# Kernel optimization log

Measured on AMD Instinct MI355X. Metric: run time of the kernel, lower is better.

Reference implementation:

```python
import jax, jax.numpy as jnp
import numpy as np

BN_EPS = 1e-5

def _batchnorm(x):
    # BatchNorm1d(affine=False) in training mode: per-feature batch stats, biased var
    mu = jnp.mean(x, axis=0, keepdims=True)
    var = jnp.mean((x - mu) ** 2, axis=0, keepdims=True)
    return (x - mu) / jnp.sqrt(var + BN_EPS)

def setup_inputs() -> dict:
    key = jax.random.key(0)
    ks = jax.random.split(key, 8)
    H, I, S, E = 1024, 4096, 128, 16384  # hidden, intermediate, sqrt(experts), experts
    std = 0.02
    return {
        "hidden_states": jax.random.normal(ks[0], (4, 2048, H), jnp.float32),
        "gate_proj_weight": jax.random.normal(ks[1], (I, H), jnp.float32) * std,
        "up_proj_weight": jax.random.normal(ks[2], (I, H), jnp.float32) * std,
        "down_proj_weight": jax.random.normal(ks[3], (H, I), jnp.float32) * std,
        "router_gate_x_weight": jax.random.normal(ks[4], (S, H), jnp.float32) * std,
        "router_gate_y_weight": jax.random.normal(ks[5], (S, H), jnp.float32) * std,
        "up_embed": jax.random.normal(ks[6], (E, H), jnp.float32) * std,
        "down_embed": jax.random.normal(ks[7], (E, H), jnp.float32) * std,
        "top_k": 16,
    }

def reference(hidden_states, gate_proj_weight, up_proj_weight, down_proj_weight,
              router_gate_x_weight, router_gate_y_weight, up_embed, down_embed, top_k):
    bsz, seq_len, H = hidden_states.shape
    x = hidden_states.reshape(-1, H)  # [T, H]
    S = router_gate_x_weight.shape[0]  # num_expert_sqrt

    # dual-axis router: two small gates -> batchnorm -> log-softmax
    lpx = jax.nn.log_softmax(_batchnorm(x @ router_gate_x_weight.T), axis=-1)  # [T, S]
    lpy = jax.nn.log_softmax(_batchnorm(x @ router_gate_y_weight.T), axis=-1)  # [T, S]
    # combined log-prob over S*S experts: expert (i,j) -> i*S + j
    combined = (lpx[:, :, None] + lpy[:, None, :]).reshape(-1, S * S)  # [T, S*S]
    scores, indices = jax.lax.top_k(combined, top_k)  # [T, K]
    routing_weights = jnp.exp(scores)  # [T, K] = p_x * p_y

    # embedding-based expert: gather up/down rows, dot-scale-combine
    ue = up_embed[indices]    # [T, K, H]
    de = down_embed[indices]  # [T, K, H]
    up_score = jnp.einsum('tkh,th->tk', ue, x)          # per-expert scalar
    experts_states = jnp.einsum('tk,tkh->th', routing_weights * up_score, de)

    # dense SwiGLU MLP branch
    mlp = (jax.nn.silu(x @ gate_proj_weight.T) * (x @ up_proj_weight.T)) @ down_proj_weight.T

    out = mlp + experts_states
    return out.reshape(bsz, seq_len, H)
```

## Files before the change

### kernel.cpp

```cpp
#include <hip/hip_runtime.h>
#include <hip/hip_bf16.h>
#include <math.h>

#define T_TOK 8192
#define HDIM  1024
#define IDIM  4096
#define SDIM  128
#define TOPK  16

typedef __bf16 bf16x8 __attribute__((ext_vector_type(8)));
typedef float  f32x4  __attribute__((ext_vector_type(4)));

__device__ __forceinline__ unsigned short f2bf(float f) {
    union { float f; unsigned u; } a; a.f = f;
    unsigned r = a.u + 0x7fffu + ((a.u >> 16) & 1u);
    return (unsigned short)(r >> 16);
}
__device__ __forceinline__ float bf2f(unsigned short b) {
    union { unsigned u; float f; } a; a.u = ((unsigned)b) << 16;
    return a.f;
}

__device__ __forceinline__ void gld_lds16(const void* g, void* l) {
    __builtin_amdgcn_global_load_lds(
        (__attribute__((address_space(1))) void*)g,
        (__attribute__((address_space(3))) void*)l,
        16, 0, 0);
}

struct CvtSegs {
    const float4* src[8];
    ushort4*      dst[8];
    int           end[8];
};

__global__ __launch_bounds__(256)
void cvt_all_kernel(CvtSegs segs) {
    int i = blockIdx.x * 256 + threadIdx.x;
    if (i >= segs.end[7]) return;
    int s = 0;
    #pragma unroll
    for (int k = 0; k < 7; ++k) s += (i >= segs.end[k]) ? 1 : 0;
    int base = (s == 0) ? 0 : segs.end[s - 1];
    int j = i - base;
    float4 v = segs.src[s][j];
    ushort4 o;
    o.x = f2bf(v.x); o.y = f2bf(v.y); o.z = f2bf(v.z); o.w = f2bf(v.w);
    segs.dst[s][j] = o;
}

template<int ADD>
__global__ __launch_bounds__(256)
void gemm_bt(const unsigned short* __restrict__ A, const unsigned short* __restrict__ B,
             float* __restrict__ C, int M, int N, int K) {
    __shared__ unsigned short As[4096];
    __shared__ unsigned short Bs[4096];
    const int tid  = threadIdx.x;
    const int lane = tid & 63;
    const int wave = tid >> 6;
    const int tm = blockIdx.x * 128;
    const int tn = blockIdx.y * 128;
    const int wm = (wave & 1) * 64;
    const int wn = (wave >> 1) * 64;
    const int quad = lane >> 4;
    const int tr   = lane & 15;

    f32x4 acc[4][4] = {};
    bf16x8 af[4], bfr[4];

    const int ua0 = tid,        am0 = ua0 & 127, ak0 = ua0 >> 7;
    const int ua1 = tid + 256,  am1 = ua1 & 127, ak1 = ua1 >> 7;

    auto issue = [&](int kt) {
        gld_lds16(A + (size_t)(tm + am0) * K + kt + ak0 * 8, &As[ua0 * 8]);
        gld_lds16(A + (size_t)(tm + am1) * K + kt + ak1 * 8, &As[ua1 * 8]);
        gld_lds16(B + (size_t)(tn + am0) * K + kt + ak0 * 8, &Bs[ua0 * 8]);
        gld_lds16(B + (size_t)(tn + am1) * K + kt + ak1 * 8, &Bs[ua1 * 8]);
    };
    auto rdfrags = [&]() {
        #pragma unroll
        for (int mi = 0; mi < 4; ++mi)
            af[mi] = *(const bf16x8*)&As[(quad * 128 + wm + mi * 16 + tr) * 8];
        #pragma unroll
        for (int ni = 0; ni < 4; ++ni)
            bfr[ni] = *(const bf16x8*)&Bs[(quad * 128 + wn + ni * 16 + tr) * 8];
    };
    auto mfmas = [&]() {
        #pragma unroll
        for (int mi = 0; mi < 4; ++mi)
            #pragma unroll
            for (int ni = 0; ni < 4; ++ni)
                acc[mi][ni] = __builtin_amdgcn_mfma_f32_16x16x32_bf16(af[mi], bfr[ni], acc[mi][ni], 0, 0, 0);
    };

    issue(0);
    asm volatile("s_waitcnt vmcnt(0)" ::: "memory");
    __syncthreads();
    rdfrags();
    for (int kt = 32; kt < K; kt += 32) {
        __syncthreads();
        issue(kt);
        mfmas();
        asm volatile("s_waitcnt vmcnt(0)" ::: "memory");
        __syncthreads();
        rdfrags();
    }
    mfmas();

    #pragma unroll
    for (int mi = 0; mi < 4; ++mi) {
        #pragma unroll
        for (int ni = 0; ni < 4; ++ni) {
            int col = tn + wn + ni * 16 + tr;
            #pragma unroll
            for (int r = 0; r < 4; ++r) {
                int row = tm + wm + mi * 16 + quad * 4 + r;
                size_t o = (size_t)row * N + col;
                float v = acc[mi][ni][r];
                if (ADD) v += C[o];
                C[o] = v;
            }
        }
    }
}

#define BARX() asm volatile("s_barrier" ::: "memory")
#define VMW4() asm volatile("s_waitcnt vmcnt(4)" ::: "memory")
#define VMW3() asm volatile("s_waitcnt vmcnt(3)" ::: "memory")

#define RD_A(par, ks, MB) { const char* _p = lds + ((par) << 15) + ((ks) << 14); \
    af[0] = *(const bf16x8*)(_p + aoff[(MB)+0]); \
    af[1] = *(const bf16x8*)(_p + aoff[(MB)+1]); \
    af[2] = *(const bf16x8*)(_p + aoff[(MB)+2]); \
    af[3] = *(const bf16x8*)(_p + aoff[(MB)+3]); }

#define RD_B(par, ks) { const char* _p = lds + 65536 + ((par) << 15) + ((ks) << 14); \
    bfv[0] = *(const bf16x8*)(_p + boff[0]); \
    bfv[1] = *(const bf16x8*)(_p + boff[1]); \
    bfv[2] = *(const bf16x8*)(_p + boff[2]); \
    bfv[3] = *(const bf16x8*)(_p + boff[3]); }

#define MMA16(ACC) { __builtin_amdgcn_s_setprio(1); \
    _Pragma("unroll") \
    for (int _i = 0; _i < 4; ++_i) \
        _Pragma("unroll") \
        for (int _n = 0; _n < 4; ++_n) \
            ACC[_i][_n] = __builtin_amdgcn_mfma_f32_16x16x32_bf16(af[_i], bfv[_n], ACC[_i][_n], 0, 0, 0); \
    __builtin_amdgcn_s_setprio(0); }

__global__ __launch_bounds__(512, 2)
void gemm1_8ph(const unsigned short* __restrict__ Xb, const unsigned short* __restrict__ Wg,
               const unsigned short* __restrict__ Wu, unsigned short* __restrict__ Hb) {
    __shared__ __align__(16) char lds[131072];
    const int tid  = threadIdx.x;
    const int lane = tid & 63;
    const int wid  = tid >> 6;
    const int quad = lane >> 4;
    const int tr   = lane & 15;
    const int wm   = (wid >> 2) << 7;
    const int wn   = (wid & 3) << 6;

    const int bid = blockIdx.x;
    const int swz = (bid & 7) * 128 + (bid >> 3);
    const int gm  = (swz & 31) << 8;
    const int gn  = (swz >> 5) << 8;

    const int vsw  = (tid & 7) ^ ((tid >> 3) & 7);
    const int rowb = ((tid >> 3) << 1) | (vsw >> 2);
    const int cq8  = (vsw & 3) << 3;

    const unsigned short* pA0 = Xb + (size_t)(gm + rowb) * HDIM + cq8;
    const unsigned short* pA1 = pA0 + (size_t)128 * HDIM;
    auto wsrc = [&](int R) -> const unsigned short* {
        const unsigned short* base = ((R >> 4) & 1) ? Wu : Wg;
        int sr = ((R >> 5) << 4) | (R & 15);
        return base + (size_t)sr * HDIM + cq8;
    };
    const unsigned short* pB0 = wsrc(gn + rowb);
    const unsigned short* pB1 = wsrc(gn + rowb + 128);

    int aoff[8], boff[4];
    #pragma unroll
    for (int i = 0; i < 8; ++i) {
        int row = wm + i * 16 + tr;
        aoff[i] = ((row >> 1) << 7) | (((((row & 1) << 2) | quad) ^ ((row >> 1) & 7)) << 4);
    }
    #pragma unroll
    for (int i = 0; i < 4; ++i) {
        int row = wn + i * 16 + tr;
        boff[i] = ((row >> 1) << 7) | (((((row & 1) << 2) | quad) ^ ((row >> 1) & 7)) << 4);
    }

    f32x4 accL[4][4] = {};
    f32x4 accH[4][4] = {};
    bf16x8 af[4], bfv[4];

    auto stageA = [&](int nxt, int ks, int kOff) {
        char* d = lds + (nxt << 15) + (ks << 14) + (tid << 4);
        gld_lds16(pA0 + kOff, d);
        gld_lds16(pA1 + kOff, d + 8192);
    };
    auto stageB = [&](int nxt, int ks, int kOff) {
        char* d = lds + 65536 + (nxt << 15) + (ks << 14) + (tid << 4);
        gld_lds16(pB0 + kOff, d);
        gld_lds16(pB1 + kOff, d + 8192);
    };

    stageA(0, 0, 0);  stageB(0, 0, 0);
    stageA(0, 1, 32); stageB(0, 1, 32);
    asm volatile("s_waitcnt vmcnt(0)" ::: "memory");
    BARX();

    for (int t = 0; t < 16; ++t) {
        const int par = t & 1, nxt = par ^ 1;
        const int kN = (t < 15 ? t + 1 : 15) << 6;
        RD_A(par, 0, 0); RD_B(par, 0);
        stageA(nxt, 0, kN);
        BARX();
        MMA16(accL);
        BARX();
        RD_A(par, 0, 4);
        stageB(nxt, 0, kN);
        VMW4(); BARX();
        MMA16(accH);
        BARX();
        RD_A(par, 1, 0); RD_B(par, 1);
        stageA(nxt, 1, kN + 32);
        BARX();
        MMA16(accL);
        BARX();
        RD_A(par, 1, 4);
        stageB(nxt, 1, kN + 32);
        VMW4(); BARX();
        MMA16(accH);
        BARX();
    }
    asm volatile("s_waitcnt vmcnt(0)" ::: "memory");

    const size_t icb = (size_t)((gn + wn) >> 1) + tr;
    const int rbase = gm + wm + quad * 4;
    #pragma unroll
    for (int mi = 0; mi < 4; ++mi) {
        #pragma unroll
        for (int p = 0; p < 2; ++p) {
            #pragma unroll
            for (int r = 0; r < 4; ++r) {
                {
                    float g = accL[mi][2 * p][r], u = accL[mi][2 * p + 1][r];
                    float h = g / (1.0f + __expf(-g)) * u;
                    Hb[(size_t)(rbase + mi * 16 + r) * IDIM + icb + 16 * p] = f2bf(h);
                }
                {
                    float g = accH[mi][2 * p][r], u = accH[mi][2 * p + 1][r];
                    float h = g / (1.0f + __expf(-g)) * u;
                    Hb[(size_t)(rbase + 64 + mi * 16 + r) * IDIM + icb + 16 * p] = f2bf(h);
                }
            }
        }
    }
}

#define RD2_A(par, ks) { const char* _p = lds + ((par) << 15) + ((ks) << 14); \
    _Pragma("unroll") \
    for (int _i = 0; _i < 8; ++_i) af[_i] = *(const bf16x8*)(_p + aoff[_i]); }

#define RD2_B(par, ks) { const char* _p = lds + 65536 + ((par) << 14) + ((ks) << 13); \
    bfv[0] = *(const bf16x8*)(_p + boff[0]); \
    bfv[1] = *(const bf16x8*)(_p + boff[1]); }

#define MMA2() { __builtin_amdgcn_s_setprio(1); \
    _Pragma("unroll") \
    for (int _i = 0; _i < 8; ++_i) \
        _Pragma("unroll") \
        for (int _n = 0; _n < 2; ++_n) \
            acc[_i][_n] = __builtin_amdgcn_mfma_f32_16x16x32_bf16(af[_i], bfv[_n], acc[_i][_n], 0, 0, 0); \
    __builtin_amdgcn_s_setprio(0); }

__global__ __launch_bounds__(512, 2)
void gemm2_8ph(const unsigned short* __restrict__ A, const unsigned short* __restrict__ B,
               float* __restrict__ C) {
    __shared__ __align__(16) char lds[98304];
    const int K = IDIM, N = HDIM;
    const int tid  = threadIdx.x;
    const int lane = tid & 63;
    const int wid  = tid >> 6;
    const int quad = lane >> 4;
    const int tr   = lane & 15;
    const int wm   = (wid >> 2) << 7;
    const int wn   = (wid & 3) << 5;

    const int bid = blockIdx.x;
    const int swz = (bid & 7) * 32 + (bid >> 3);
    const int gm  = (swz & 31) << 8;
    const int gn  = (swz >> 5) << 7;

    const int vsw  = (tid & 7) ^ ((tid >> 3) & 7);
    const int rowb = ((tid >> 3) << 1) | (vsw >> 2);
    const int cq8  = (vsw & 3) << 3;

    const unsigned short* pA0 = A + (size_t)(gm + rowb) * K + cq8;
    const unsigned short* pA1 = pA0 + (size_t)128 * K;
    const unsigned short* pB0 = B + (size_t)(gn + rowb) * K + cq8;

    int aoff[8], boff[2];
    #pragma unroll
    for (int i = 0; i < 8; ++i) {
        int row = wm + i * 16 + tr;
        aoff[i] = ((row >> 1) << 7) | (((((row & 1) << 2) | quad) ^ ((row >> 1) & 7)) << 4);
    }
    #pragma unroll
    for (int i = 0; i < 2; ++i) {
        int row = wn + i * 16 + tr;
        boff[i] = ((row >> 1) << 7) | (((((row & 1) << 2) | quad) ^ ((row >> 1) & 7)) << 4);
    }

    f32x4 acc[8][2] = {};
    bf16x8 af[8], bfv[2];

    auto stageA = [&](int nxt, int ks, int kOff) {
        char* d = lds + (nxt << 15) + (ks << 14) + (tid << 4);
        gld_lds16(pA0 + kOff, d);
        gld_lds16(pA1 + kOff, d + 8192);
    };
    auto stageB = [&](int nxt, int ks, int kOff) {
        char* d = lds + 65536 + (nxt << 14) + (ks << 13) + (tid << 4);
        gld_lds16(pB0 + kOff, d);
    };

    stageA(0, 0, 0); stageB(0, 0, 0);
    stageA(0, 1, 32); stageB(0, 1, 32);
    asm volatile("s_waitcnt vmcnt(0)" ::: "memory");
    BARX();

    for (int t = 0; t < 64; ++t) {
        const int par = t & 1, nxt = par ^ 1;
        const int kN = (t < 63 ? t + 1 : 63) << 6;
        RD2_A(par, 0); RD2_B(par, 0);
        stageA(nxt, 0, kN); stageB(nxt, 0, kN);
        VMW3(); BARX();
        MMA2();
        BARX();
        RD2_A(par, 1); RD2_B(par, 1);
        stageA(nxt, 1, kN + 32); stageB(nxt, 1, kN + 32);
        VMW3(); BARX();
        MMA2();
        BARX();
    }
    asm volatile("s_waitcnt vmcnt(0)" ::: "memory");

    #pragma unroll
    for (int mi = 0; mi < 8; ++mi) {
        #pragma unroll
        for (int ni = 0; ni < 2; ++ni) {
            int col = gn + wn + ni * 16 + tr;
            #pragma unroll
            for (int r = 0; r < 4; ++r) {
                int row = gm + wm + mi * 16 + quad * 4 + r;
                size_t o = (size_t)row * N + col;
                C[o] += acc[mi][ni][r];
            }
        }
    }
}

__global__ void bn_stats(const float* __restrict__ gxy, float* __restrict__ sums, float* __restrict__ ssq) {
    const int j = threadIdx.x;
    const int b = blockIdx.x;
    float s = 0.f, q = 0.f;
    for (int r = 0; r < 32; ++r) {
        float v = gxy[(size_t)(b * 32 + r) * 256 + j];
        s += v; q += v * v;
    }
    atomicAdd(&sums[j], s);
    atomicAdd(&ssq[j], q);
}

__global__ __launch_bounds__(256)
void routing_kernel(const float* __restrict__ gxy, const float* __restrict__ sums,
                    const float* __restrict__ ssq, int* __restrict__ oidx, float* __restrict__ owt) {
    const int lane = threadIdx.x & 63;
    const int t = blockIdx.x * 4 + (threadIdx.x >> 6);
    const float invT = 1.0f / (float)T_TOK;
    const float* g = gxy + (size_t)t * 256;

    float z[4];
    const int cols[4] = {lane, lane + 64, 128 + lane, 192 + lane};
    #pragma unroll
    for (int i = 0; i < 4; ++i) {
        int c = cols[i];
        float mu  = sums[c] * invT;
        float var = ssq[c] * invT - mu * mu;
        z[i] = (g[c] - mu) * rsqrtf(var + 1e-5f);
    }
    float mx = fmaxf(z[0], z[1]);
    float my = fmaxf(z[2], z[3]);
    #pragma unroll
    for (int m = 32; m >= 1; m >>= 1) {
        mx = fmaxf(mx, __shfl_xor(mx, m));
        my = fmaxf(my, __shfl_xor(my, m));
    }
    float sx = __expf(z[0] - mx) + __expf(z[1] - mx);
    float sy = __expf(z[2] - my) + __expf(z[3] - my);
    #pragma unroll
    for (int m = 32; m >= 1; m >>= 1) {
        sx += __shfl_xor(sx, m);
        sy += __shfl_xor(sy, m);
    }
    float lx0 = z[0] - (mx + __logf(sx)), lx1 = z[1] - (mx + __logf(sx));
    float ly0 = z[2] - (my + __logf(sy)), ly1 = z[3] - (my + __logf(sy));

    float aw = -INFINITY; int ai = 0;
    float bw = -INFINITY; int bi = 0;
    {
        float v0 = lx0, v1 = lx1;
        for (int i = 0; i < 16; ++i) {
            float v; int c;
            if (v0 >= v1) { v = v0; c = lane; } else { v = v1; c = lane + 64; }
            #pragma unroll
            for (int m = 32; m >= 1; m >>= 1) {
                float ov = __shfl_xor(v, m); int oc = __shfl_xor(c, m);
                if (ov > v || (ov == v && oc < c)) { v = ov; c = oc; }
            }
            if ((c & 63) == lane) { if (c < 64) v0 = -INFINITY; else v1 = -INFINITY; }
            if (lane == i) { aw = v; ai = c; }
        }
    }
    {
        float v0 = ly0, v1 = ly1;
        for (int i = 0; i < 16; ++i) {
            float v; int c;
            if (v0 >= v1) { v = v0; c = lane; } else { v = v1; c = lane + 64; }
            #pragma unroll
            for (int m = 32; m >= 1; m >>= 1) {
                float ov = __shfl_xor(v, m); int oc = __shfl_xor(c, m);
                if (ov > v || (ov == v && oc < c)) { v = ov; c = oc; }
            }
            if ((c & 63) == lane) { if (c < 64) v0 = -INFINITY; else v1 = -INFINITY; }
            if (lane == i) { bw = v; bi = c; }
        }
    }
    float cv[4];
    #pragma unroll
    for (int j = 0; j < 4; ++j) {
        int c = lane + 64 * j;
        cv[j] = __shfl(aw, c >> 4) + __shfl(bw, c & 15);
    }
    int myidx = 0; float myw = 0.f;
    for (int i = 0; i < 16; ++i) {
        float v = cv[0]; int c = lane;
        #pragma unroll
        for (int j = 1; j < 4; ++j) { int cc = lane + 64 * j; if (cv[j] > v) { v = cv[j]; c = cc; } }
        #pragma unroll
        for (int m = 32; m >= 1; m >>= 1) {
            float ov = __shfl_xor(v, m); int oc = __shfl_xor(c, m);
            if (ov > v || (ov == v && oc < c)) { v = ov; c = oc; }
        }
        #pragma unroll
        for (int j = 0; j < 4; ++j) if (c == lane + 64 * j) cv[j] = -INFINITY;
        int p = c >> 4, q = c & 15;
        int ex = __shfl(ai, p);
        int ey = __shfl(bi, q);
        if (lane == i) { myidx = ex * 128 + ey; myw = __expf(v); }
    }
    if (lane < 16) {
        oidx[t * TOPK + lane] = myidx;
        owt[t * TOPK + lane]  = myw;
    }
}

__global__ __launch_bounds__(256)
void expert_combine(const unsigned short* __restrict__ xb, const int* __restrict__ idx,
                    const float* __restrict__ wts, const unsigned short* __restrict__ ueb,
                    const unsigned short* __restrict__ deb, float* __restrict__ out) {
    const int t = blockIdx.x;
    const int tid = threadIdx.x;
    const int lane = tid & 63, wv = tid >> 6;
    __shared__ float part[TOPK * 4];
    __shared__ float sc[TOPK];
    ushort4 xv4 = ((const ushort4*)(xb + (size_t)t * HDIM))[tid];
    float x0 = bf2f(xv4.x), x1 = bf2f(xv4.y), x2 = bf2f(xv4.z), x3 = bf2f(xv4.w);
    int e[TOPK];
    #pragma unroll
    for (int k = 0; k < TOPK; ++k) e[k] = idx[t * TOPK + k];
    #pragma unroll
    for (int k = 0; k < TOPK; ++k) {
        ushort4 u4 = ((const ushort4*)(ueb + (size_t)e[k] * HDIM))[tid];
        float p = bf2f(u4.x) * x0 + bf2f(u4.y) * x1 + bf2f(u4.z) * x2 + bf2f(u4.w) * x3;
        #pragma unroll
        for (int m = 32; m >= 1; m >>= 1) p += __shfl_xor(p, m);
        if (lane == 0) part[k * 4 + wv] = p;
    }
    __syncthreads();
    if (tid < TOPK) {
        float s = part[tid * 4] + part[tid * 4 + 1] + part[tid * 4 + 2] + part[tid * 4 + 3];
        sc[tid] = s * wts[t * TOPK + tid];
    }
    __syncthreads();
    float4 acc = {0.f, 0.f, 0.f, 0.f};
    #pragma unroll
    for (int k = 0; k < TOPK; ++k) {
        float s = sc[k];
        ushort4 d4 = ((const ushort4*)(deb + (size_t)e[k] * HDIM))[tid];
        acc.x += s * bf2f(d4.x); acc.y += s * bf2f(d4.y);
        acc.z += s * bf2f(d4.z); acc.w += s * bf2f(d4.w);
    }
    ((float4*)(out + (size_t)t * HDIM))[tid] = acc;
}

extern "C" void kernel_launch(void* const* d_in, const int* in_sizes, int n_in,
                              void* d_out, int out_size, void* d_ws, size_t ws_size,
                              hipStream_t stream) {
    const float* x  = (const float*)d_in[0];
    const float* gw = (const float*)d_in[1];
    const float* uw = (const float*)d_in[2];
    const float* dw = (const float*)d_in[3];
    const float* wx = (const float*)d_in[4];
    const float* wy = (const float*)d_in[5];
    const float* ue = (const float*)d_in[6];
    const float* de = (const float*)d_in[7];
    float* out = (float*)d_out;

    char* ws = (char*)d_ws;
    size_t o = 0;
    auto alloc = [&](size_t bytes) { void* p = ws + o; o += (bytes + 255) & ~(size_t)255; return p; };
    unsigned short* xb    = (unsigned short*)alloc((size_t)T_TOK * HDIM * 2);
    unsigned short* gateb = (unsigned short*)alloc((size_t)IDIM * HDIM * 2);
    unsigned short* upb   = (unsigned short*)alloc((size_t)IDIM * HDIM * 2);
    unsigned short* downb = (unsigned short*)alloc((size_t)HDIM * IDIM * 2);
    unsigned short* wrb   = (unsigned short*)alloc((size_t)256 * HDIM * 2);
    unsigned short* ueb   = (unsigned short*)alloc((size_t)16384 * HDIM * 2);
    unsigned short* deb   = (unsigned short*)alloc((size_t)16384 * HDIM * 2);
    unsigned short* hbuf  = (unsigned short*)alloc((size_t)T_TOK * IDIM * 2);
    float* gxy  = (float*)alloc((size_t)T_TOK * 256 * 4);
    float* sums = (float*)alloc(256 * 4);
    float* ssq  = (float*)alloc(256 * 4);
    int*   idxs = (int*)alloc((size_t)T_TOK * TOPK * 4);
    float* wts  = (float*)alloc((size_t)T_TOK * TOPK * 4);

    CvtSegs segs;
    const float* srcs[8] = {x, gw, uw, dw, wx, wy, ue, de};
    unsigned short* dsts[8] = {xb, gateb, upb, downb, wrb, wrb + SDIM * HDIM, ueb, deb};
    const int cnt4[8] = {T_TOK * HDIM / 4, IDIM * HDIM / 4, IDIM * HDIM / 4, IDIM * HDIM / 4,
                         SDIM * HDIM / 4, SDIM * HDIM / 4, 16384 * HDIM / 4, 16384 * HDIM / 4};
    int acc = 0;
    for (int i = 0; i < 8; ++i) {
        segs.src[i] = (const float4*)srcs[i];
        segs.dst[i] = (ushort4*)dsts[i];
        acc += cnt4[i];
        segs.end[i] = acc;
    }
    cvt_all_kernel<<<(acc + 255) / 256, 256, 0, stream>>>(segs);

    hipMemsetAsync(sums, 0, 2 * 256 * 4, stream);
    gemm_bt<0><<<dim3(T_TOK / 128, 256 / 128), 256, 0, stream>>>(xb, wrb, gxy, T_TOK, 256, HDIM);
    bn_stats<<<256, 256, 0, stream>>>(gxy, sums, ssq);
    routing_kernel<<<T_TOK / 4, 256, 0, stream>>>(gxy, sums, ssq, idxs, wts);

    expert_combine<<<T_TOK, 256, 0, stream>>>(xb, idxs, wts, ueb, deb, out);

    gemm1_8ph<<<1024, 512, 0, stream>>>(xb, gateb, upb, hbuf);
    gemm2_8ph<<<256, 512, 0, stream>>>(hbuf, downb, out);
}
```

Measured before the change: 690.4 us.

## Use four-slot ring buffer with deeper prefetch in both GEMM kernels

Replaces the double-buffered (two k-halves per parity) LDS staging with a 4-slot ring of 32-wide K chunks, prefetching three chunks ahead instead of one. The vmcnt waits are relaxed so more global-to-LDS loads stay in flight, hiding memory latency. The block-to-tile swizzle is also changed in both kernels to alter L2 locality of A/B tiles. Adds more outstanding loads and changes wait counts, which risks correctness if counts are off.

```diff
diff --git a/kernel.cpp b/kernel.cpp
--- a/kernel.cpp
+++ b/kernel.cpp
@@ -125,16 +125,15 @@
 }
 
 #define BARX() asm volatile("s_barrier" ::: "memory")
-#define VMW4() asm volatile("s_waitcnt vmcnt(4)" ::: "memory")
-#define VMW3() asm volatile("s_waitcnt vmcnt(3)" ::: "memory")
-
-#define RD_A(par, ks, MB) { const char* _p = lds + ((par) << 15) + ((ks) << 14); \
+#define VMW(n) asm volatile("s_waitcnt vmcnt(" #n ")" ::: "memory")
+
+#define RD_A(r, MB) { const char* _p = lds + ((r) << 14); \
     af[0] = *(const bf16x8*)(_p + aoff[(MB)+0]); \
     af[1] = *(const bf16x8*)(_p + aoff[(MB)+1]); \
     af[2] = *(const bf16x8*)(_p + aoff[(MB)+2]); \
     af[3] = *(const bf16x8*)(_p + aoff[(MB)+3]); }
 
-#define RD_B(par, ks) { const char* _p = lds + 65536 + ((par) << 15) + ((ks) << 14); \
+#define RD_B(r) { const char* _p = lds + 65536 + ((r) << 14); \
     bfv[0] = *(const bf16x8*)(_p + boff[0]); \
     bfv[1] = *(const bf16x8*)(_p + boff[1]); \
     bfv[2] = *(const bf16x8*)(_p + boff[2]); \
@@ -161,9 +160,9 @@
     const int wn   = (wid & 3) << 6;
 
     const int bid = blockIdx.x;
-    const int swz = (bid & 7) * 128 + (bid >> 3);
-    const int gm  = (swz & 31) << 8;
-    const int gn  = (swz >> 5) << 8;
+    const int u   = bid >> 3;
+    const int gm  = (((bid & 7) << 2) | (u & 3)) << 8;
+    const int gn  = (u >> 2) << 8;
 
     const int vsw  = (tid & 7) ^ ((tid >> 3) & 7);
     const int rowb = ((tid >> 3) << 1) | (vsw >> 2);
@@ -195,43 +194,34 @@
     f32x4 accH[4][4] = {};
     bf16x8 af[4], bfv[4];
 
-    auto stageA = [&](int nxt, int ks, int kOff) {
-        char* d = lds + (nxt << 15) + (ks << 14) + (tid << 4);
+    auto stageA = [&](int slot, int kOff) {
+        char* d = lds + (slot << 14) + (tid << 4);
         gld_lds16(pA0 + kOff, d);
         gld_lds16(pA1 + kOff, d + 8192);
     };
-    auto stageB = [&](int nxt, int ks, int kOff) {
-        char* d = lds + 65536 + (nxt << 15) + (ks << 14) + (tid << 4);
+    auto stageB = [&](int slot, int kOff) {
+        char* d = lds + 65536 + (slot << 14) + (tid << 4);
         gld_lds16(pB0 + kOff, d);
         gld_lds16(pB1 + kOff, d + 8192);
     };
 
-    stageA(0, 0, 0);  stageB(0, 0, 0);
-    stageA(0, 1, 32); stageB(0, 1, 32);
-    asm volatile("s_waitcnt vmcnt(0)" ::: "memory");
-    BARX();
-
-    for (int t = 0; t < 16; ++t) {
-        const int par = t & 1, nxt = par ^ 1;
-        const int kN = (t < 15 ? t + 1 : 15) << 6;
-        RD_A(par, 0, 0); RD_B(par, 0);
-        stageA(nxt, 0, kN);
+    stageA(0, 0);  stageB(0, 0);
+    stageA(1, 32); stageB(1, 32);
+    stageA(2, 64); stageB(2, 64);
+    VMW(8); BARX();
+
+    for (int t = 0; t < 32; ++t) {
+        const int r  = t & 3;
+        const int rn = (t + 3) & 3;
+        const int kN = (t < 29 ? t + 3 : 31) << 5;
+        RD_A(r, 0); RD_B(r);
+        stageA(rn, kN);
         BARX();
         MMA16(accL);
         BARX();
-        RD_A(par, 0, 4);
-        stageB(nxt, 0, kN);
-        VMW4(); BARX();
-        MMA16(accH);
-        BARX();
-        RD_A(par, 1, 0); RD_B(par, 1);
-        stageA(nxt, 1, kN + 32);
-        BARX();
-        MMA16(accL);
-        BARX();
-        RD_A(par, 1, 4);
-        stageB(nxt, 1, kN + 32);
-        VMW4(); BARX();
+        RD_A(r, 4);
+        stageB(rn, kN);
+        VMW(8); BARX();
         MMA16(accH);
         BARX();
     }
@@ -246,13 +236,13 @@
             #pragma unroll
             for (int r = 0; r < 4; ++r) {
                 {
-                    float g = accL[mi][2 * p][r], u = accL[mi][2 * p + 1][r];
-                    float h = g / (1.0f + __expf(-g)) * u;
+                    float g = accL[mi][2 * p][r], u2 = accL[mi][2 * p + 1][r];
+                    float h = g / (1.0f + __expf(-g)) * u2;
                     Hb[(size_t)(rbase + mi * 16 + r) * IDIM + icb + 16 * p] = f2bf(h);
                 }
                 {
-                    float g = accH[mi][2 * p][r], u = accH[mi][2 * p + 1][r];
-                    float h = g / (1.0f + __expf(-g)) * u;
+                    float g = accH[mi][2 * p][r], u2 = accH[mi][2 * p + 1][r];
+                    float h = g / (1.0f + __expf(-g)) * u2;
                     Hb[(size_t)(rbase + 64 + mi * 16 + r) * IDIM + icb + 16 * p] = f2bf(h);
                 }
             }
@@ -260,11 +250,11 @@
     }
 }
 
-#define RD2_A(par, ks) { const char* _p = lds + ((par) << 15) + ((ks) << 14); \
+#define RD2_A(r) { const char* _p = lds + ((r) << 14); \
     _Pragma("unroll") \
     for (int _i = 0; _i < 8; ++_i) af[_i] = *(const bf16x8*)(_p + aoff[_i]); }
 
-#define RD2_B(par, ks) { const char* _p = lds + 65536 + ((par) << 14) + ((ks) << 13); \
+#define RD2_B(r) { const char* _p = lds + 65536 + ((r) << 13); \
     bfv[0] = *(const bf16x8*)(_p + boff[0]); \
     bfv[1] = *(const bf16x8*)(_p + boff[1]); }
 
@@ -290,9 +280,9 @@
     const int wn   = (wid & 3) << 5;
 
     const int bid = blockIdx.x;
-    const int swz = (bid & 7) * 32 + (bid >> 3);
-    const int gm  = (swz & 31) << 8;
-    const int gn  = (swz >> 5) << 7;
+    const int u   = bid >> 3;
+    const int gm  = (((bid & 7) << 2) | (u >> 3)) << 8;
+    const int gn  = (u & 7) << 7;
 
     const int vsw  = (tid & 7) ^ ((tid >> 3) & 7);
     const int rowb = ((tid >> 3) << 1) | (vsw >> 2);
@@ -317,32 +307,28 @@
     f32x4 acc[8][2] = {};
     bf16x8 af[8], bfv[2];
 
-    auto stageA = [&](int nxt, int ks, int kOff) {
-        char* d = lds + (nxt << 15) + (ks << 14) + (tid << 4);
+    auto stageA = [&](int slot, int kOff) {
+        char* d = lds + (slot << 14) + (tid << 4);
         gld_lds16(pA0 + kOff, d);
         gld_lds16(pA1 + kOff, d + 8192);
     };
-    auto stageB = [&](int nxt, int ks, int kOff) {
-        char* d = lds + 65536 + (nxt << 14) + (ks << 13) + (tid << 4);
+    auto stageB = [&](int slot, int kOff) {
+        char* d = lds + 65536 + (slot << 13) + (tid << 4);
         gld_lds16(pB0 + kOff, d);
     };
 
-    stageA(0, 0, 0); stageB(0, 0, 0);
-    stageA(0, 1, 32); stageB(0, 1, 32);
-    asm volatile("s_waitcnt vmcnt(0)" ::: "memory");
-    BARX();
-
-    for (int t = 0; t < 64; ++t) {
-        const int par = t & 1, nxt = par ^ 1;
-        const int kN = (t < 63 ? t + 1 : 63) << 6;
-        RD2_A(par, 0); RD2_B(par, 0);
-        stageA(nxt, 0, kN); stageB(nxt, 0, kN);
-        VMW3(); BARX();
-        MMA2();
-        BARX();
-        RD2_A(par, 1); RD2_B(par, 1);
-        stageA(nxt, 1, kN + 32); stageB(nxt, 1, kN + 32);
-        VMW3(); BARX();
+    stageA(0, 0);  stageB(0, 0);
+    stageA(1, 32); stageB(1, 32);
+    stageA(2, 64); stageB(2, 64);
+    VMW(6); BARX();
+
+    for (int t = 0; t < 128; ++t) {
+        const int r  = t & 3;
+        const int rn = (t + 3) & 3;
+        const int kN = (t < 125 ? t + 3 : 127) << 5;
+        RD2_A(r); RD2_B(r);
+        stageA(rn, kN); stageB(rn, kN);
+        VMW(6); BARX();
         MMA2();
         BARX();
     }
```

Result: faster. 634.8 us (-8.1%).
